# Kernel optimization log

Measured on AMD Instinct MI355X. Metric: run time of the kernel, lower is better.

Reference implementation:

```python
import jax, jax.numpy as jnp
import numpy as np

H = 128  # hidden_size
I = 28   # input_size
C = 10   # num_classes


def setup_inputs() -> dict:
    key = jax.random.key(0)
    ks = jax.random.split(key, 11)
    s = 1.0 / np.sqrt(H)  # torch nn.RNN init scale
    return {
        "x": jax.random.normal(ks[0], (8192, 28, I), dtype=jnp.float32),
        "W_ih0": jax.random.uniform(ks[1], (H, I), jnp.float32, -s, s),
        "W_hh0": jax.random.uniform(ks[2], (H, H), jnp.float32, -s, s),
        "b_ih0": jax.random.uniform(ks[3], (H,), jnp.float32, -s, s),
        "b_hh0": jax.random.uniform(ks[4], (H,), jnp.float32, -s, s),
        "W_ih1": jax.random.uniform(ks[5], (H, H), jnp.float32, -s, s),
        "W_hh1": jax.random.uniform(ks[6], (H, H), jnp.float32, -s, s),
        "b_ih1": jax.random.uniform(ks[7], (H,), jnp.float32, -s, s),
        "b_hh1": jax.random.uniform(ks[8], (H,), jnp.float32, -s, s),
        "fc_w": jax.random.uniform(ks[9], (C, H), jnp.float32, -s, s),
        "fc_b": jax.random.uniform(ks[10], (C,), jnp.float32, -s, s),
    }


def _rnn_layer_full(x, W_ih, b_ih, W_hh, b_hh):
    # x: [B, T, D] -> full output sequence [B, T, H]
    B = x.shape[0]
    h0 = jnp.zeros((B, H), x.dtype)
    xw = jnp.einsum('btd,hd->bth', x, W_ih) + b_ih  # precompute input GEMM

    def step(h, xw_t):
        h = jnp.tanh(xw_t + h @ W_hh.T + b_hh)
        return h, h

    _, ys = jax.lax.scan(step, h0, jnp.swapaxes(xw, 0, 1))  # [T, B, H]
    return jnp.swapaxes(ys, 0, 1)


def _rnn_layer_last(x, W_ih, b_ih, W_hh, b_hh):
    # only the final hidden state is needed downstream
    B = x.shape[0]
    h0 = jnp.zeros((B, H), x.dtype)
    xw = jnp.einsum('btd,hd->bth', x, W_ih) + b_ih

    def step(h, xw_t):
        h = jnp.tanh(xw_t + h @ W_hh.T + b_hh)
        return h, None

    h_last, _ = jax.lax.scan(step, h0, jnp.swapaxes(xw, 0, 1))
    return h_last


def reference(x, W_ih0, W_hh0, b_ih0, b_hh0, W_ih1, W_hh1, b_ih1, b_hh1, fc_w, fc_b):
    out0 = _rnn_layer_full(x, W_ih0, b_ih0, W_hh0, b_hh0)   # [B, T, H]
    h_last = _rnn_layer_last(out0, W_ih1, b_ih1, W_hh1, b_hh1)  # [B, H] == out[:, -1, :]
    return h_last @ fc_w.T + fc_b  # [B, C]
```

## Files before the change

### kernel.cpp

```cpp
#include <hip/hip_runtime.h>

#define HSZ 128
#define ISZ 28
#define TSZ 28
#define CSZ 10
#define BT  16
#define NT  512
#define HP  136
#define XP  32

typedef _Float16 half_t;
typedef _Float16 v8h __attribute__((ext_vector_type(8)));
typedef _Float16 v4h __attribute__((ext_vector_type(4)));
typedef float v4f __attribute__((ext_vector_type(4)));

__device__ __forceinline__ float fast_tanh(float x) {
    float e = __expf(2.f * x);
    return 1.f - 2.f * __builtin_amdgcn_rcpf(e + 1.f);
}

__global__ __launch_bounds__(NT, 4)
void rnn_mfma3(const float* __restrict__ x,
               const float* __restrict__ W_ih0, const float* __restrict__ W_hh0,
               const float* __restrict__ b_ih0, const float* __restrict__ b_hh0,
               const float* __restrict__ W_ih1, const float* __restrict__ W_hh1,
               const float* __restrict__ b_ih1, const float* __restrict__ b_hh1,
               const float* __restrict__ fc_w, const float* __restrict__ fc_b,
               float* __restrict__ out)
{
    __shared__ half_t h0s[2][BT * HP];
    __shared__ half_t h1s[2][BT * HP];
    __shared__ half_t xss[2][BT * XP];

    const int tid  = threadIdx.x;
    const int wave = tid >> 6;
    const int lane = tid & 63;
    const int ln   = lane & 15;
    const int quad = lane >> 4;
    const int kq   = quad * 8;
    const int b0   = blockIdx.x * BT;
    const int base = wave * 16;
    const int row  = base + ln;

    v8h aWx, aW0[4], aW1i[4], aW1h[4];
    v4f bias0, bias1;
    {
        float4 p = *(const float4*)(b_ih0 + base + quad * 4);
        float4 q = *(const float4*)(b_hh0 + base + quad * 4);
        bias0 = (v4f){p.x + q.x, p.y + q.y, p.z + q.z, p.w + q.w};
        p = *(const float4*)(b_ih1 + base + quad * 4);
        q = *(const float4*)(b_hh1 + base + quad * 4);
        bias1 = (v4f){p.x + q.x, p.y + q.y, p.z + q.z, p.w + q.w};
    }
    {
        const float* pw = W_ih0 + row * ISZ + kq;
        float4 a = *(const float4*)pw;
        float4 b = (kq < 24) ? *(const float4*)(pw + 4) : make_float4(0.f, 0.f, 0.f, 0.f);
        aWx = (v8h){(half_t)a.x, (half_t)a.y, (half_t)a.z, (half_t)a.w,
                    (half_t)b.x, (half_t)b.y, (half_t)b.z, (half_t)b.w};
    }
#pragma unroll
    for (int ks = 0; ks < 4; ++ks) {
        const float4* p0 = (const float4*)(W_hh0 + row * HSZ + ks * 32 + kq);
        const float4* p1 = (const float4*)(W_ih1 + row * HSZ + ks * 32 + kq);
        const float4* p2 = (const float4*)(W_hh1 + row * HSZ + ks * 32 + kq);
        float4 a = p0[0], b = p0[1];
        aW0[ks] = (v8h){(half_t)a.x, (half_t)a.y, (half_t)a.z, (half_t)a.w,
                        (half_t)b.x, (half_t)b.y, (half_t)b.z, (half_t)b.w};
        a = p1[0]; b = p1[1];
        aW1i[ks] = (v8h){(half_t)a.x, (half_t)a.y, (half_t)a.z, (half_t)a.w,
                         (half_t)b.x, (half_t)b.y, (half_t)b.z, (half_t)b.w};
        a = p2[0]; b = p2[1];
        aW1h[ks] = (v8h){(half_t)a.x, (half_t)a.y, (half_t)a.z, (half_t)a.w,
                         (half_t)b.x, (half_t)b.y, (half_t)b.z, (half_t)b.w};
    }

    const int  xm  = tid >> 5;
    const int  xi  = tid & 31;
    const bool xok = xi < ISZ;
    const float* xrow = x + (size_t)(b0 + xm) * (TSZ * ISZ) + xi;

    xss[0][xm * XP + xi] = (half_t)(xok ? xrow[0] : 0.f);
    xss[1][xm * XP + xi] = (half_t)(xok ? xrow[ISZ] : 0.f);
    float xcur = xok ? xrow[2 * ISZ] : 0.f;

    for (int idx = tid; idx < BT * HP; idx += NT)
        h1s[0][idx] = (half_t)0.f;
    __syncthreads();

    {
        const v8h bx = *(const v8h*)&xss[0][ln * XP + kq];
        v4f a0 = bias0;
        a0 = __builtin_amdgcn_mfma_f32_16x16x32_f16(aWx, bx, a0, 0, 0, 0);
        v4h p = {(half_t)fast_tanh(a0[0]), (half_t)fast_tanh(a0[1]),
                 (half_t)fast_tanh(a0[2]), (half_t)fast_tanh(a0[3])};
        *(v4h*)&h0s[0][ln * HP + base + quad * 4] = p;
    }
    __syncthreads();

    for (int t = 0; t < TSZ - 1; ++t) {
        const int pr = t & 1;

        float xnew = 0.f;
        if (t < TSZ - 3 && xok) xnew = xrow[(t + 3) * ISZ];

        v8h bh0[4];
#pragma unroll
        for (int ks = 0; ks < 4; ++ks)
            bh0[ks] = *(const v8h*)&h0s[pr][ln * HP + ks * 32 + kq];
        const v8h bx = *(const v8h*)&xss[pr ^ 1][ln * XP + kq];

        v4f a1 = bias1, a0 = bias0;
        a0 = __builtin_amdgcn_mfma_f32_16x16x32_f16(aWx, bx, a0, 0, 0, 0);
#pragma unroll
        for (int ks = 0; ks < 4; ++ks) {
            const v8h bh1 = *(const v8h*)&h1s[pr][ln * HP + ks * 32 + kq];
            a1 = __builtin_amdgcn_mfma_f32_16x16x32_f16(aW1i[ks], bh0[ks], a1, 0, 0, 0);
            a1 = __builtin_amdgcn_mfma_f32_16x16x32_f16(aW1h[ks], bh1,     a1, 0, 0, 0);
            a0 = __builtin_amdgcn_mfma_f32_16x16x32_f16(aW0[ks],  bh0[ks], a0, 0, 0, 0);
        }

        {
            v4h p1 = {(half_t)fast_tanh(a1[0]), (half_t)fast_tanh(a1[1]),
                      (half_t)fast_tanh(a1[2]), (half_t)fast_tanh(a1[3])};
            *(v4h*)&h1s[pr ^ 1][ln * HP + base + quad * 4] = p1;
            v4h p0 = {(half_t)fast_tanh(a0[0]), (half_t)fast_tanh(a0[1]),
                      (half_t)fast_tanh(a0[2]), (half_t)fast_tanh(a0[3])};
            *(v4h*)&h0s[pr ^ 1][ln * HP + base + quad * 4] = p0;
        }

        if (t < TSZ - 2)
            xss[pr][xm * XP + xi] = (half_t)xcur;
        xcur = xnew;

        __syncthreads();
    }

    {
        const int pr = (TSZ - 1) & 1;
        v4f a1 = bias1;
#pragma unroll
        for (int ks = 0; ks < 4; ++ks) {
            const v8h bh0 = *(const v8h*)&h0s[pr][ln * HP + ks * 32 + kq];
            const v8h bh1 = *(const v8h*)&h1s[pr][ln * HP + ks * 32 + kq];
            a1 = __builtin_amdgcn_mfma_f32_16x16x32_f16(aW1i[ks], bh0, a1, 0, 0, 0);
            a1 = __builtin_amdgcn_mfma_f32_16x16x32_f16(aW1h[ks], bh1, a1, 0, 0, 0);
        }
        v4h p1 = {(half_t)fast_tanh(a1[0]), (half_t)fast_tanh(a1[1]),
                  (half_t)fast_tanh(a1[2]), (half_t)fast_tanh(a1[3])};
        *(v4h*)&h1s[pr ^ 1][ln * HP + base + quad * 4] = p1;
    }
    __syncthreads();

    if (tid < BT * CSZ) {
        const int m = tid / CSZ, cc = tid - m * CSZ;
        float s = fc_b[cc];
#pragma unroll
        for (int k8 = 0; k8 < HSZ / 8; ++k8) {
            const v8h hv = *(const v8h*)&h1s[0][m * HP + k8 * 8];
            const float4 w0 = *(const float4*)(fc_w + cc * HSZ + k8 * 8);
            const float4 w1 = *(const float4*)(fc_w + cc * HSZ + k8 * 8 + 4);
            s += (float)hv[0] * w0.x + (float)hv[1] * w0.y +
                 (float)hv[2] * w0.z + (float)hv[3] * w0.w +
                 (float)hv[4] * w1.x + (float)hv[5] * w1.y +
                 (float)hv[6] * w1.z + (float)hv[7] * w1.w;
        }
        out[(b0 + m) * CSZ + cc] = s;
    }
}

extern "C" void kernel_launch(void* const* d_in, const int* in_sizes, int n_in,
                              void* d_out, int out_size, void* d_ws, size_t ws_size,
                              hipStream_t stream) {
    const float* x     = (const float*)d_in[0];
    const float* W_ih0 = (const float*)d_in[1];
    const float* W_hh0 = (const float*)d_in[2];
    const float* b_ih0 = (const float*)d_in[3];
    const float* b_hh0 = (const float*)d_in[4];
    const float* W_ih1 = (const float*)d_in[5];
    const float* W_hh1 = (const float*)d_in[6];
    const float* b_ih1 = (const float*)d_in[7];
    const float* b_hh1 = (const float*)d_in[8];
    const float* fc_w  = (const float*)d_in[9];
    const float* fc_b  = (const float*)d_in[10];
    float* out = (float*)d_out;

    const int B = in_sizes[0] / (TSZ * ISZ);
    dim3 grid(B / BT), block(NT);
    rnn_mfma3<<<grid, block, 0, stream>>>(x, W_ih0, W_hh0, b_ih0, b_hh0,
                                          W_ih1, W_hh1, b_ih1, b_hh1,
                                          fc_w, fc_b, out);
}
```

Baseline: 127.3 us.

## Split MFMA accumulators into independent chains and unroll recurrence loop by two

Each step's MFMA chain now runs on two independent accumulators per layer (c/d), summed before tanh. Along with interleaved LDS loads, this shortens the serial dependency chain within a timestep. The time loop is unrolled by two with a compile-time buffer parity. The x prefetch becomes branch-free by clamping indices (masking padded weights to zero), and the x tile row pitch grows to 40 to reduce LDS bank conflicts. The cost is extra vector adds and a few more registers per step.

Result: no change. 128.4 us (+0.9%).

```diff
diff --git a/kernel.cpp b/kernel.cpp
--- a/kernel.cpp
+++ b/kernel.cpp
@@ -7,7 +7,7 @@
 #define BT  16
 #define NT  512
 #define HP  136
-#define XP  32
+#define XP  40
 
 typedef _Float16 half_t;
 typedef _Float16 v8h __attribute__((ext_vector_type(8)));
@@ -20,7 +20,7 @@
 }
 
 __global__ __launch_bounds__(NT, 4)
-void rnn_mfma3(const float* __restrict__ x,
+void rnn_mfma5(const float* __restrict__ x,
                const float* __restrict__ W_ih0, const float* __restrict__ W_hh0,
                const float* __restrict__ b_ih0, const float* __restrict__ b_hh0,
                const float* __restrict__ W_ih1, const float* __restrict__ W_hh1,
@@ -57,7 +57,8 @@
         float4 a = *(const float4*)pw;
         float4 b = (kq < 24) ? *(const float4*)(pw + 4) : make_float4(0.f, 0.f, 0.f, 0.f);
         aWx = (v8h){(half_t)a.x, (half_t)a.y, (half_t)a.z, (half_t)a.w,
-                    (half_t)b.x, (half_t)b.y, (half_t)b.z, (half_t)b.w};
+                    (half_t)(kq + 4 < ISZ ? b.x : 0.f), (half_t)(kq + 5 < ISZ ? b.y : 0.f),
+                    (half_t)(kq + 6 < ISZ ? b.z : 0.f), (half_t)(kq + 7 < ISZ ? b.w : 0.f)};
     }
 #pragma unroll
     for (int ks = 0; ks < 4; ++ks) {
@@ -75,14 +76,14 @@
                          (half_t)b.x, (half_t)b.y, (half_t)b.z, (half_t)b.w};
     }
 
-    const int  xm  = tid >> 5;
-    const int  xi  = tid & 31;
-    const bool xok = xi < ISZ;
-    const float* xrow = x + (size_t)(b0 + xm) * (TSZ * ISZ) + xi;
-
-    xss[0][xm * XP + xi] = (half_t)(xok ? xrow[0] : 0.f);
-    xss[1][xm * XP + xi] = (half_t)(xok ? xrow[ISZ] : 0.f);
-    float xcur = xok ? xrow[2 * ISZ] : 0.f;
+    const int xm = tid >> 5;
+    const int xi = tid & 31;
+    const int xiC = xi < ISZ ? xi : ISZ - 1;
+    const float* xrow = x + (size_t)(b0 + xm) * (TSZ * ISZ) + xiC;
+
+    xss[0][xm * XP + xi] = (half_t)xrow[0];
+    xss[1][xm * XP + xi] = (half_t)xrow[ISZ];
+    float xc = xrow[2 * ISZ];
 
     for (int idx = tid; idx < BT * HP; idx += NT)
         h1s[0][idx] = (half_t)0.f;
@@ -98,57 +99,73 @@
     }
     __syncthreads();
 
-    for (int t = 0; t < TSZ - 1; ++t) {
-        const int pr = t & 1;
-
-        float xnew = 0.f;
-        if (t < TSZ - 3 && xok) xnew = xrow[(t + 3) * ISZ];
-
-        v8h bh0[4];
-#pragma unroll
-        for (int ks = 0; ks < 4; ++ks)
-            bh0[ks] = *(const v8h*)&h0s[pr][ln * HP + ks * 32 + kq];
+    auto seg = [&](int t, int pr, bool doX) __attribute__((always_inline)) {
+        int tn = t + 3; if (tn > TSZ - 1) tn = TSZ - 1;
+        const float xn = xrow[tn * ISZ];
+
+        v8h bh0_0 = *(const v8h*)&h0s[pr][ln * HP + 0 * 32 + kq];
+        v8h bh0_1 = *(const v8h*)&h0s[pr][ln * HP + 1 * 32 + kq];
+        v8h bh0_2 = *(const v8h*)&h0s[pr][ln * HP + 2 * 32 + kq];
+        v8h bh0_3 = *(const v8h*)&h0s[pr][ln * HP + 3 * 32 + kq];
         const v8h bx = *(const v8h*)&xss[pr ^ 1][ln * XP + kq];
 
-        v4f a1 = bias1, a0 = bias0;
-        a0 = __builtin_amdgcn_mfma_f32_16x16x32_f16(aWx, bx, a0, 0, 0, 0);
-#pragma unroll
-        for (int ks = 0; ks < 4; ++ks) {
-            const v8h bh1 = *(const v8h*)&h1s[pr][ln * HP + ks * 32 + kq];
-            a1 = __builtin_amdgcn_mfma_f32_16x16x32_f16(aW1i[ks], bh0[ks], a1, 0, 0, 0);
-            a1 = __builtin_amdgcn_mfma_f32_16x16x32_f16(aW1h[ks], bh1,     a1, 0, 0, 0);
-            a0 = __builtin_amdgcn_mfma_f32_16x16x32_f16(aW0[ks],  bh0[ks], a0, 0, 0, 0);
-        }
-
-        {
-            v4h p1 = {(half_t)fast_tanh(a1[0]), (half_t)fast_tanh(a1[1]),
-                      (half_t)fast_tanh(a1[2]), (half_t)fast_tanh(a1[3])};
-            *(v4h*)&h1s[pr ^ 1][ln * HP + base + quad * 4] = p1;
-            v4h p0 = {(half_t)fast_tanh(a0[0]), (half_t)fast_tanh(a0[1]),
-                      (half_t)fast_tanh(a0[2]), (half_t)fast_tanh(a0[3])};
-            *(v4h*)&h0s[pr ^ 1][ln * HP + base + quad * 4] = p0;
-        }
-
-        if (t < TSZ - 2)
-            xss[pr][xm * XP + xi] = (half_t)xcur;
-        xcur = xnew;
-
-        __syncthreads();
-    }
-
-    {
-        const int pr = (TSZ - 1) & 1;
-        v4f a1 = bias1;
-#pragma unroll
-        for (int ks = 0; ks < 4; ++ks) {
-            const v8h bh0 = *(const v8h*)&h0s[pr][ln * HP + ks * 32 + kq];
-            const v8h bh1 = *(const v8h*)&h1s[pr][ln * HP + ks * 32 + kq];
-            a1 = __builtin_amdgcn_mfma_f32_16x16x32_f16(aW1i[ks], bh0, a1, 0, 0, 0);
-            a1 = __builtin_amdgcn_mfma_f32_16x16x32_f16(aW1h[ks], bh1, a1, 0, 0, 0);
-        }
+        v4f c0 = bias0, d0 = (v4f){0.f, 0.f, 0.f, 0.f};
+        v4f c1 = bias1, d1 = (v4f){0.f, 0.f, 0.f, 0.f};
+
+        c0 = __builtin_amdgcn_mfma_f32_16x16x32_f16(aWx,      bx,    c0, 0, 0, 0);
+        c1 = __builtin_amdgcn_mfma_f32_16x16x32_f16(aW1i[0],  bh0_0, c1, 0, 0, 0);
+        v8h bh1_0 = *(const v8h*)&h1s[pr][ln * HP + 0 * 32 + kq];
+        d1 = __builtin_amdgcn_mfma_f32_16x16x32_f16(aW1h[0],  bh1_0, d1, 0, 0, 0);
+        c0 = __builtin_amdgcn_mfma_f32_16x16x32_f16(aW0[0],   bh0_0, c0, 0, 0, 0);
+        d0 = __builtin_amdgcn_mfma_f32_16x16x32_f16(aW0[1],   bh0_1, d0, 0, 0, 0);
+        c1 = __builtin_amdgcn_mfma_f32_16x16x32_f16(aW1i[1],  bh0_1, c1, 0, 0, 0);
+        v8h bh1_1 = *(const v8h*)&h1s[pr][ln * HP + 1 * 32 + kq];
+        d1 = __builtin_amdgcn_mfma_f32_16x16x32_f16(aW1h[1],  bh1_1, d1, 0, 0, 0);
+        c0 = __builtin_amdgcn_mfma_f32_16x16x32_f16(aW0[2],   bh0_2, c0, 0, 0, 0);
+        d0 = __builtin_amdgcn_mfma_f32_16x16x32_f16(aW0[3],   bh0_3, d0, 0, 0, 0);
+        c1 = __builtin_amdgcn_mfma_f32_16x16x32_f16(aW1i[2],  bh0_2, c1, 0, 0, 0);
+        v8h bh1_2 = *(const v8h*)&h1s[pr][ln * HP + 2 * 32 + kq];
+        d1 = __builtin_amdgcn_mfma_f32_16x16x32_f16(aW1h[2],  bh1_2, d1, 0, 0, 0);
+        c1 = __builtin_amdgcn_mfma_f32_16x16x32_f16(aW1i[3],  bh0_3, c1, 0, 0, 0);
+        v8h bh1_3 = *(const v8h*)&h1s[pr][ln * HP + 3 * 32 + kq];
+        d1 = __builtin_amdgcn_mfma_f32_16x16x32_f16(aW1h[3],  bh1_3, d1, 0, 0, 0);
+
+        const v4f a0 = c0 + d0;
+        const v4f a1 = c1 + d1;
+
         v4h p1 = {(half_t)fast_tanh(a1[0]), (half_t)fast_tanh(a1[1]),
                   (half_t)fast_tanh(a1[2]), (half_t)fast_tanh(a1[3])};
         *(v4h*)&h1s[pr ^ 1][ln * HP + base + quad * 4] = p1;
+        v4h p0 = {(half_t)fast_tanh(a0[0]), (half_t)fast_tanh(a0[1]),
+                  (half_t)fast_tanh(a0[2]), (half_t)fast_tanh(a0[3])};
+        *(v4h*)&h0s[pr ^ 1][ln * HP + base + quad * 4] = p0;
+
+        if (doX)
+            xss[pr][xm * XP + xi] = (half_t)xc;
+        xc = xn;
+
+        __syncthreads();
+    };
+
+    for (int tp = 0; tp < 13; ++tp) {
+        seg(2 * tp,     0, true);
+        seg(2 * tp + 1, 1, true);
+    }
+    seg(26, 0, false);
+
+    {
+        v4f c1 = bias1, d1 = (v4f){0.f, 0.f, 0.f, 0.f};
+#pragma unroll
+        for (int ks = 0; ks < 4; ++ks) {
+            const v8h bh0 = *(const v8h*)&h0s[1][ln * HP + ks * 32 + kq];
+            const v8h bh1 = *(const v8h*)&h1s[1][ln * HP + ks * 32 + kq];
+            c1 = __builtin_amdgcn_mfma_f32_16x16x32_f16(aW1i[ks], bh0, c1, 0, 0, 0);
+            d1 = __builtin_amdgcn_mfma_f32_16x16x32_f16(aW1h[ks], bh1, d1, 0, 0, 0);
+        }
+        const v4f a1 = c1 + d1;
+        v4h p1 = {(half_t)fast_tanh(a1[0]), (half_t)fast_tanh(a1[1]),
+                  (half_t)fast_tanh(a1[2]), (half_t)fast_tanh(a1[3])};
+        *(v4h*)&h1s[0][ln * HP + base + quad * 4] = p1;
     }
     __syncthreads();
 
@@ -187,7 +204,7 @@
 
     const int B = in_sizes[0] / (TSZ * ISZ);
     dim3 grid(B / BT), block(NT);
-    rnn_mfma3<<<grid, block, 0, stream>>>(x, W_ih0, W_hh0, b_ih0, b_hh0,
+    rnn_mfma5<<<grid, block, 0, stream>>>(x, W_ih0, W_hh0, b_ih0, b_hh0,
                                           W_ih1, W_hh1, b_ih1, b_hh1,
                                           fc_w, fc_b, out);
 }
```
